# Kernel tuning notes

Hardware: AMD Instinct MI355X
Metric: run time of the kernel (lower is better)

## Reference

```python
import jax, jax.numpy as jnp
import numpy as np

CODEBOOK_SIZE = 8192
EMBED_DIM = 256


def setup_inputs() -> dict:
    key = jax.random.key(0)
    k1, k2 = jax.random.split(key)
    z = jax.random.normal(k1, (8, 4096, EMBED_DIM), dtype=jnp.float32)
    # matches torch init: uniform_(-1/codebook_size, 1/codebook_size)
    codebook = jax.random.uniform(
        k2, (CODEBOOK_SIZE, EMBED_DIM), dtype=jnp.float32,
        minval=-1.0 / CODEBOOK_SIZE, maxval=1.0 / CODEBOOK_SIZE)
    return {"z": z, "codebook": codebook}


def reference(z, codebook):
    # z: [B, S, D]; codebook: [K, D]
    z_flat = z.reshape(-1, z.shape[-1])                      # [N, D]
    # ||z||^2 - 2 z.E^T + ||E||^2  -> [N, K]
    distances = (
        jnp.sum(z_flat * z_flat, axis=1, keepdims=True)
        - 2.0 * jnp.einsum("nd,kd->nk", z_flat, codebook)
        + jnp.sum(codebook * codebook, axis=1)
    )
    encoding_indices = jnp.argmin(distances, axis=1)         # [N]
    z_q = codebook[encoding_indices].reshape(z.shape)        # [B, S, D]
    return z_q, encoding_indices
```

## Files before the change

### kernel.cpp

```cpp
#include <hip/hip_runtime.h>


#define NROWS 32768
#define DIM   256
#define KCB   8192
#define CANDCAP 128
#define MARGIN  4.5e-4f
#define WBUF    320
#define NTILE   512
#define RECB    9216

#define OFF_CAND  0
#define OFF_CNT   2097152
#define OFF_ZSQ   2129920
#define OFF_CSQ   2162688
#define OFF_OVL   2170880
#define OFF_OVC   2203648
#define OFF_IMG   2203664
#define OFF_IDX   8388608

using bf16x8 = __attribute__((ext_vector_type(8))) short;
using f32x4  = __attribute__((ext_vector_type(4))) float;

__device__ __forceinline__ unsigned short bf16rne(float f) {
    unsigned u = __float_as_uint(f);
    unsigned r = u + 0x7FFFu + ((u >> 16) & 1u);
    return (unsigned short)(r >> 16);
}

__device__ __forceinline__ void gld_lds16(const void* g, void* l) {
    __builtin_amdgcn_global_load_lds(
        (const __attribute__((address_space(1))) void*)g,
        (__attribute__((address_space(3))) void*)l, 16, 0, 0);
}

__device__ float np_sumsq_256(const float* __restrict__ p) {
#pragma clang fp contract(off)
    float blk[2];
    #pragma unroll
    for (int b = 0; b < 2; ++b) {
        const float* q = p + b * 128;
        float r[8];
        #pragma unroll
        for (int j = 0; j < 8; ++j) r[j] = __fmul_rn(q[j], q[j]);
        for (int i = 8; i < 128; i += 8) {
            #pragma unroll
            for (int j = 0; j < 8; ++j)
                r[j] = __fadd_rn(r[j], __fmul_rn(q[i + j], q[i + j]));
        }
        blk[b] = __fadd_rn(
            __fadd_rn(__fadd_rn(r[0], r[1]), __fadd_rn(r[2], r[3])),
            __fadd_rn(__fadd_rn(r[4], r[5]), __fadd_rn(r[6], r[7])));
    }
    return __fadd_rn(blk[0], blk[1]);
}

__global__ void vq_sumsq2_kernel(const float* __restrict__ z,
                                 const float* __restrict__ cb,
                                 float* __restrict__ zsq, float* __restrict__ csq) {
    int r = blockIdx.x * 256 + threadIdx.x;
    if (r < NROWS) zsq[r] = np_sumsq_256(z + (size_t)r * DIM);
    else if (r < NROWS + KCB) csq[r - NROWS] = np_sumsq_256(cb + (size_t)(r - NROWS) * DIM);
}

__global__ void vq_prepB_kernel(const float* __restrict__ cb,
                                const float* __restrict__ csq,
                                char* __restrict__ img,
                                unsigned* __restrict__ cnt, unsigned* __restrict__ ovc) {
    int t = blockIdx.x * 256 + threadIdx.x;
    if (t < NROWS) cnt[t] = 0;
    if (t == 0) *ovc = 0;
    if (t < 262144) {
        int s = t & 63, kk = (t >> 6) & 7, T = t >> 9;
        int code = T * 16 + (s >> 2), lhi = s & 3;
        const float* src = cb + (size_t)code * DIM + kk * 32 + lhi * 8;
        float4 v0 = *reinterpret_cast<const float4*>(src);
        float4 v1 = *reinterpret_cast<const float4*>(src + 4);
        uint4 o;
        o.x = (unsigned)bf16rne(v0.x) | ((unsigned)bf16rne(v0.y) << 16);
        o.y = (unsigned)bf16rne(v0.z) | ((unsigned)bf16rne(v0.w) << 16);
        o.z = (unsigned)bf16rne(v1.x) | ((unsigned)bf16rne(v1.y) << 16);
        o.w = (unsigned)bf16rne(v1.z) | ((unsigned)bf16rne(v1.w) << 16);
        *reinterpret_cast<uint4*>(img + (size_t)T * RECB + kk * 1024 + s * 16) = o;
    } else {
        int t2 = t - 262144;
        if (t2 < NTILE * 4) {
            int T = t2 >> 2, q = t2 & 3;
            float4 c = *reinterpret_cast<const float4*>(&csq[T * 16 + q * 4]);
            c.x += 1.0f; c.y += 1.0f; c.z += 1.0f; c.w += 1.0f;
            *reinterpret_cast<float4*>(img + (size_t)T * RECB + 8192 + q * 16) = c;
        }
    }
}

__global__ __launch_bounds__(512, 1) void vq_screen_kernel(
    const float* __restrict__ z, const char* __restrict__ img,
    unsigned* __restrict__ cnt, unsigned short* __restrict__ cand) {
    __shared__ __align__(16) unsigned char Bpriv[8][2][RECB];
    __shared__ unsigned runmin[128];
    __shared__ unsigned wcnt[8];
    __shared__ unsigned wbuf[8][WBUF];
    const int tid = threadIdx.x, lane = tid & 63, wid = tid >> 6;
    const int wr = wid >> 2, wc = wid & 3;
    const int l15 = lane & 15, lhi = lane >> 4;
    const int row0 = blockIdx.x * 128;
    const int tbase = wc * 128;
    unsigned char* myB = &Bpriv[wid][0][0];

    bf16x8 ah[4][8];
    #pragma unroll
    for (int m = 0; m < 4; ++m) {
        const float* zr = z + (size_t)(row0 + wr * 64 + m * 16 + l15) * DIM;
        #pragma unroll
        for (int kk = 0; kk < 8; ++kk) {
            float4 v0 = *reinterpret_cast<const float4*>(zr + kk * 32 + lhi * 8);
            float4 v1 = *reinterpret_cast<const float4*>(zr + kk * 32 + lhi * 8 + 4);
            uint4 o;
            o.x = (unsigned)bf16rne(v0.x) | ((unsigned)bf16rne(v0.y) << 16);
            o.y = (unsigned)bf16rne(v0.z) | ((unsigned)bf16rne(v0.w) << 16);
            o.z = (unsigned)bf16rne(v1.x) | ((unsigned)bf16rne(v1.y) << 16);
            o.w = (unsigned)bf16rne(v1.z) | ((unsigned)bf16rne(v1.w) << 16);
            ah[m][kk] = __builtin_bit_cast(bf16x8, o);
        }
    }

    if (tid < 128) runmin[tid] = 0x7F800000u;
    if (tid < 8) wcnt[tid] = 0;
    __syncthreads();

    f32x4 acc[4];
    #pragma unroll
    for (int m = 0; m < 4; ++m) acc[m] = (f32x4){0.f, 0.f, 0.f, 0.f};

    auto STAGE = [&](int buf, int ct) {
        const char* g = img + (size_t)(tbase + ct) * RECB + lane * 16;
        unsigned char* l = myB + buf * RECB;
        #pragma unroll
        for (int i = 0; i < 9; ++i)
            gld_lds16(g + i * 1024, l + i * 1024);
    };

    auto PUSH = [&](int lr, int code) {
        unsigned pi = atomicAdd(&wcnt[wid], 1u);
        if (pi < WBUF) wbuf[wid][pi] = ((unsigned)lr << 13) | (unsigned)code;
        else {
            int grow = row0 + lr;
            unsigned gs = atomicAdd(&cnt[grow], 1u);
            if (gs < CANDCAP) cand[(size_t)grow * CANDCAP + gs] = (unsigned short)code;
        }
    };

    STAGE(0, 0);

    for (int ct = 0; ct < 128; ++ct) {
        const int buf = ct & 1;
        if (ct < 127) {
            STAGE(buf ^ 1, ct + 1);
            asm volatile("s_waitcnt vmcnt(9)" ::: "memory");
        } else {
            asm volatile("s_waitcnt vmcnt(0)" ::: "memory");
        }
        const unsigned char* mb = myB + buf * RECB;
        const float cs1 = *reinterpret_cast<const float*>(mb + 8192 + l15 * 4);
        __builtin_amdgcn_s_setprio(1);
        #pragma unroll
        for (int kk = 0; kk < 8; ++kk) {
            bf16x8 bh = *reinterpret_cast<const bf16x8*>(mb + kk * 1024 + l15 * 64 + lhi * 16);
            #pragma unroll
            for (int m = 0; m < 4; ++m)
                acc[m] = __builtin_amdgcn_mfma_f32_16x16x32_bf16(ah[m][kk], bh, acc[m], 0, 0, 0);
        }
        __builtin_amdgcn_s_setprio(0);

        const int codeb = (tbase + ct) * 16 + l15;
        if (ct == 0) {
            #pragma unroll
            for (int m = 0; m < 4; ++m) {
                const int lr0 = wr * 64 + m * 16 + lhi * 4;
                #pragma unroll
                for (int r = 0; r < 4; ++r) {
                    float s2 = fmaf(acc[m][r], -2.0f, cs1);
                    float sm = s2;
                    sm = fminf(sm, __shfl_xor(sm, 1));
                    sm = fminf(sm, __shfl_xor(sm, 2));
                    sm = fminf(sm, __shfl_xor(sm, 4));
                    sm = fminf(sm, __shfl_xor(sm, 8));
                    if (l15 == 0) atomicMin(&runmin[lr0 + r], __float_as_uint(sm));
                    if (s2 < sm + MARGIN) PUSH(lr0 + r, codeb);
                }
                acc[m] = (f32x4){0.f, 0.f, 0.f, 0.f};
            }
        } else {
            #pragma unroll
            for (int m = 0; m < 4; ++m) {
                const int lr0 = wr * 64 + m * 16 + lhi * 4;
                uint4 rmb = *reinterpret_cast<const uint4*>(&runmin[lr0]);
                #pragma unroll
                for (int r = 0; r < 4; ++r) {
                    float s2 = fmaf(acc[m][r], -2.0f, cs1);
                    const unsigned rmu = (r == 0) ? rmb.x : (r == 1) ? rmb.y
                                        : (r == 2) ? rmb.z : rmb.w;
                    const float rm = __uint_as_float(rmu);
                    const bool cf = s2 < rm + MARGIN;
                    if (__any(cf)) {
                        if (cf) {
                            if (s2 < rm) atomicMin(&runmin[lr0 + r], __float_as_uint(s2));
                            PUSH(lr0 + r, codeb);
                        }
                    }
                }
                acc[m] = (f32x4){0.f, 0.f, 0.f, 0.f};
            }
        }
    }

    unsigned n = wcnt[wid]; if (n > WBUF) n = WBUF;
    for (unsigned e = lane; e < n; e += 64) {
        unsigned u = wbuf[wid][e];
        int row = row0 + (int)(u >> 13);
        int code = (int)(u & 8191u);
        unsigned slot = atomicAdd(&cnt[row], 1u);
        if (slot < CANDCAP) cand[(size_t)row * CANDCAP + slot] = (unsigned short)code;
    }
}

__global__ __launch_bounds__(256) void vq_exact_kernel(
    const float* __restrict__ z, const float* __restrict__ cb,
    const float* __restrict__ zsq, const float* __restrict__ csq,
    const unsigned* __restrict__ cnt, const unsigned short* __restrict__ cand,
    unsigned* __restrict__ ovl, unsigned* __restrict__ ovc,
    float* __restrict__ idxF) {
    __shared__ float zrow[4][DIM];
    const int wid = threadIdx.x >> 6, lane = threadIdx.x & 63;
    const int row = blockIdx.x * 4 + wid;

    float4 zv4 = *reinterpret_cast<const float4*>(&z[(size_t)row * DIM + lane * 4]);
    *reinterpret_cast<float4*>(&zrow[wid][lane * 4]) = zv4;
    __syncthreads();

    const unsigned c = cnt[row];
    if (c == 0 || c > CANDCAP) {
        if (lane == 0) { unsigned s = atomicAdd(ovc, 1u); ovl[s] = row; }
        return;
    }

    const float Zr = zsq[row];
    const float4* cb4 = reinterpret_cast<const float4*>(cb);
    float best = 3.4e38f;
    int   bi   = 0x7FFFFFFF;

    for (int j = lane; j < (int)c; j += 64) {
        int k = cand[(size_t)row * CANDCAP + j];
        float a = 0.0f;
        #pragma unroll 8
        for (int q = 0; q < 64; ++q) {
            float4 cv = cb4[(size_t)k * 64 + q];
            float4 zv = *reinterpret_cast<const float4*>(&zrow[wid][q * 4]);
            a = fmaf(zv.x, cv.x, a); a = fmaf(zv.y, cv.y, a);
            a = fmaf(zv.z, cv.z, a); a = fmaf(zv.w, cv.w, a);
        }
        float sv = __fadd_rn(__fsub_rn(Zr, __fmul_rn(2.0f, a)), csq[k]);
        if (sv < best || (sv == best && k < bi)) { best = sv; bi = k; }
    }
    #pragma unroll
    for (int mk = 32; mk >= 1; mk >>= 1) {
        float ov = __shfl_xor(best, mk);
        int   oi = __shfl_xor(bi, mk);
        if (ov < best || (ov == best && oi < bi)) { best = ov; bi = oi; }
    }
    if (lane == 0) idxF[row] = (float)bi;
}

__global__ __launch_bounds__(256) void vq_cleanup_kernel(
    const float* __restrict__ z, const float* __restrict__ cb,
    const float* __restrict__ zsq, const float* __restrict__ csq,
    const unsigned* __restrict__ ovl, const unsigned* __restrict__ ovc,
    float* __restrict__ idxF) {
    __shared__ float zrow[DIM];
    __shared__ float wv[4]; __shared__ int wi[4];
    const int lane = threadIdx.x & 63, wid = threadIdx.x >> 6;
    const unsigned count = *ovc;
    for (unsigned w = blockIdx.x; w < count; w += gridDim.x) {
        const int row = ovl[w];
        __syncthreads();
        *reinterpret_cast<float4*>(&zrow[threadIdx.x * 4 & (DIM - 1)]) =
            *reinterpret_cast<const float4*>(&z[(size_t)row * DIM + (threadIdx.x * 4 & (DIM - 1))]);
        __syncthreads();
        const float Zr = zsq[row];
        const float4* cb4 = reinterpret_cast<const float4*>(cb);
        float best = 3.4e38f; int bi = 0x7FFFFFFF;
        for (int k = threadIdx.x; k < KCB; k += 256) {
            float a = 0.0f;
            #pragma unroll 8
            for (int q = 0; q < 64; ++q) {
                float4 cv = cb4[(size_t)k * 64 + q];
                float4 zv = *reinterpret_cast<const float4*>(&zrow[q * 4]);
                a = fmaf(zv.x, cv.x, a); a = fmaf(zv.y, cv.y, a);
                a = fmaf(zv.z, cv.z, a); a = fmaf(zv.w, cv.w, a);
            }
            float sv = __fadd_rn(__fsub_rn(Zr, __fmul_rn(2.0f, a)), csq[k]);
            if (sv < best || (sv == best && k < bi)) { best = sv; bi = k; }
        }
        #pragma unroll
        for (int mk = 32; mk >= 1; mk >>= 1) {
            float ov = __shfl_xor(best, mk);
            int   oi = __shfl_xor(bi, mk);
            if (ov < best || (ov == best && oi < bi)) { best = ov; bi = oi; }
        }
        if (lane == 0) { wv[wid] = best; wi[wid] = bi; }
        __syncthreads();
        if (threadIdx.x == 0) {
            #pragma unroll
            for (int u = 1; u < 4; ++u)
                if (wv[u] < best || (wv[u] == best && wi[u] < bi)) { best = wv[u]; bi = wi[u]; }
            idxF[row] = (float)bi;
        }
    }
}

__global__ void vq_gather_kernel(const float* __restrict__ cb,
                                 const float* __restrict__ idxF,
                                 float4* __restrict__ out4) {
    int g = blockIdx.x * blockDim.x + threadIdx.x;
    const float4* cb4 = reinterpret_cast<const float4*>(cb);
    for (int i = g; i < NROWS * 64; i += gridDim.x * blockDim.x) {
        int row = i >> 6, q = i & 63;
        int idx = (int)idxF[row];
        out4[i] = cb4[(size_t)idx * 64 + q];
    }
}

extern "C" void kernel_launch(void* const* d_in, const int* in_sizes, int n_in,
                              void* d_out, int out_size, void* d_ws, size_t ws_size,
                              hipStream_t stream) {
    const float* z  = (const float*)d_in[0];
    const float* cb = (const float*)d_in[1];
    float* out = (float*)d_out;

    unsigned short* candp = (unsigned short*)(out + OFF_CAND);
    unsigned*       cntp  = (unsigned*)(out + OFF_CNT);
    float*          zsq   = out + OFF_ZSQ;
    float*          csq   = out + OFF_CSQ;
    unsigned*       ovl   = (unsigned*)(out + OFF_OVL);
    unsigned*       ovc   = (unsigned*)(out + OFF_OVC);
    char*           img   = (char*)(out + OFF_IMG);
    float*          idxF  = out + OFF_IDX;

    vq_sumsq2_kernel<<<(NROWS + KCB) / 256, 256, 0, stream>>>(z, cb, zsq, csq);
    vq_prepB_kernel<<<1032, 256, 0, stream>>>(cb, csq, img, cntp, ovc);
    vq_screen_kernel<<<NROWS / 128, 512, 0, stream>>>(z, img, cntp, candp);
    vq_exact_kernel<<<NROWS / 4, 256, 0, stream>>>(z, cb, zsq, csq, cntp, candp, ovl, ovc, idxF);
    vq_cleanup_kernel<<<64, 256, 0, stream>>>(z, cb, zsq, csq, ovl, ovc, idxF);
    vq_gather_kernel<<<2048, 256, 0, stream>>>(cb, idxF, (float4*)out);
}
```

Measured before the change: 351.6 us.

## Load codebook tiles straight to registers and drop the LDS staging buffers

The screening kernel stops staging bf16 codebook tiles through per-wave LDS double buffers with global_load_lds. It now loads each lane's B fragments directly into registers with a two-deep register ping-pong and software-pipelined MFMA/epilogue. The image layout is reordered so that each lane's 16-byte fragment is contiguous, and csq+1 is moved to its own array. Removing roughly 147KB of LDS allows launch bounds of two blocks per CU, raising occupancy, at the cost of more VGPR pressure and no LDS reuse across waves.

```diff
diff --git a/kernel.cpp b/kernel.cpp
--- a/kernel.cpp
+++ b/kernel.cpp
@@ -8,15 +8,15 @@
 #define MARGIN  4.5e-4f
 #define WBUF    320
 #define NTILE   512
-#define RECB    9216
 
 #define OFF_CAND  0
 #define OFF_CNT   2097152
 #define OFF_ZSQ   2129920
 #define OFF_CSQ   2162688
-#define OFF_OVL   2170880
-#define OFF_OVC   2203648
-#define OFF_IMG   2203664
+#define OFF_CSQ1  2170880
+#define OFF_OVL   2179072
+#define OFF_OVC   2211840
+#define OFF_IMG   2211856
 #define OFF_IDX   8388608
 
 using bf16x8 = __attribute__((ext_vector_type(8))) short;
@@ -26,12 +26,6 @@
     unsigned u = __float_as_uint(f);
     unsigned r = u + 0x7FFFu + ((u >> 16) & 1u);
     return (unsigned short)(r >> 16);
-}
-
-__device__ __forceinline__ void gld_lds16(const void* g, void* l) {
-    __builtin_amdgcn_global_load_lds(
-        (const __attribute__((address_space(1))) void*)g,
-        (__attribute__((address_space(3))) void*)l, 16, 0, 0);
 }
 
 __device__ float np_sumsq_256(const float* __restrict__ p) {
@@ -65,15 +59,15 @@
 
 __global__ void vq_prepB_kernel(const float* __restrict__ cb,
                                 const float* __restrict__ csq,
-                                char* __restrict__ img,
+                                char* __restrict__ img, float* __restrict__ csq1,
                                 unsigned* __restrict__ cnt, unsigned* __restrict__ ovc) {
     int t = blockIdx.x * 256 + threadIdx.x;
     if (t < NROWS) cnt[t] = 0;
     if (t == 0) *ovc = 0;
     if (t < 262144) {
         int s = t & 63, kk = (t >> 6) & 7, T = t >> 9;
-        int code = T * 16 + (s >> 2), lhi = s & 3;
-        const float* src = cb + (size_t)code * DIM + kk * 32 + lhi * 8;
+        int code = s & 15, lhi = s >> 4;
+        const float* src = cb + (size_t)(T * 16 + code) * DIM + kk * 32 + lhi * 8;
         float4 v0 = *reinterpret_cast<const float4*>(src);
         float4 v1 = *reinterpret_cast<const float4*>(src + 4);
         uint4 o;
@@ -81,22 +75,16 @@
         o.y = (unsigned)bf16rne(v0.z) | ((unsigned)bf16rne(v0.w) << 16);
         o.z = (unsigned)bf16rne(v1.x) | ((unsigned)bf16rne(v1.y) << 16);
         o.w = (unsigned)bf16rne(v1.z) | ((unsigned)bf16rne(v1.w) << 16);
-        *reinterpret_cast<uint4*>(img + (size_t)T * RECB + kk * 1024 + s * 16) = o;
-    } else {
-        int t2 = t - 262144;
-        if (t2 < NTILE * 4) {
-            int T = t2 >> 2, q = t2 & 3;
-            float4 c = *reinterpret_cast<const float4*>(&csq[T * 16 + q * 4]);
-            c.x += 1.0f; c.y += 1.0f; c.z += 1.0f; c.w += 1.0f;
-            *reinterpret_cast<float4*>(img + (size_t)T * RECB + 8192 + q * 16) = c;
-        }
-    }
-}
-
-__global__ __launch_bounds__(512, 1) void vq_screen_kernel(
+        *reinterpret_cast<uint4*>(img + (size_t)T * 8192 + kk * 1024 + s * 16) = o;
+    } else if (t < 262144 + KCB) {
+        csq1[t - 262144] = csq[t - 262144] + 1.0f;
+    }
+}
+
+__global__ __launch_bounds__(512, 2) void vq_screen_kernel(
     const float* __restrict__ z, const char* __restrict__ img,
+    const float* __restrict__ csq1,
     unsigned* __restrict__ cnt, unsigned short* __restrict__ cand) {
-    __shared__ __align__(16) unsigned char Bpriv[8][2][RECB];
     __shared__ unsigned runmin[128];
     __shared__ unsigned wcnt[8];
     __shared__ unsigned wbuf[8][WBUF];
@@ -105,7 +93,6 @@
     const int l15 = lane & 15, lhi = lane >> 4;
     const int row0 = blockIdx.x * 128;
     const int tbase = wc * 128;
-    unsigned char* myB = &Bpriv[wid][0][0];
 
     bf16x8 ah[4][8];
     #pragma unroll
@@ -132,13 +119,12 @@
     #pragma unroll
     for (int m = 0; m < 4; ++m) acc[m] = (f32x4){0.f, 0.f, 0.f, 0.f};
 
-    auto STAGE = [&](int buf, int ct) {
-        const char* g = img + (size_t)(tbase + ct) * RECB + lane * 16;
-        unsigned char* l = myB + buf * RECB;
-        #pragma unroll
-        for (int i = 0; i < 9; ++i)
-            gld_lds16(g + i * 1024, l + i * 1024);
-    };
+    const char*  gp = img + (size_t)tbase * 8192 + (size_t)lane * 16;
+    const float* cp = csq1 + tbase * 16 + l15;
+    int codeb = tbase * 16 + l15;
+
+    uint4 bA[8]; float csA;
+    uint4 bB[8]; float csB;
 
     auto PUSH = [&](int lr, int code) {
         unsigned pi = atomicAdd(&wcnt[wid], 1u);
@@ -150,68 +136,87 @@
         }
     };
 
-    STAGE(0, 0);
-
-    for (int ct = 0; ct < 128; ++ct) {
-        const int buf = ct & 1;
-        if (ct < 127) {
-            STAGE(buf ^ 1, ct + 1);
-            asm volatile("s_waitcnt vmcnt(9)" ::: "memory");
-        } else {
-            asm volatile("s_waitcnt vmcnt(0)" ::: "memory");
-        }
-        const unsigned char* mb = myB + buf * RECB;
-        const float cs1 = *reinterpret_cast<const float*>(mb + 8192 + l15 * 4);
-        __builtin_amdgcn_s_setprio(1);
+#define LOADR(bh, cs)                                                     \
+    {                                                                     \
+        _Pragma("unroll")                                                 \
+        for (int kk = 0; kk < 8; ++kk)                                    \
+            bh[kk] = *reinterpret_cast<const uint4*>(gp + kk * 1024);     \
+        cs = *cp;                                                         \
+        gp += 8192; cp += 16;                                             \
+    }
+
+#define MFMAS(bh)                                                         \
+    {                                                                     \
+        __builtin_amdgcn_s_setprio(1);                                    \
+        _Pragma("unroll")                                                 \
+        for (int kk = 0; kk < 8; ++kk) {                                  \
+            bf16x8 bhv = __builtin_bit_cast(bf16x8, bh[kk]);              \
+            _Pragma("unroll")                                             \
+            for (int m = 0; m < 4; ++m)                                   \
+                acc[m] = __builtin_amdgcn_mfma_f32_16x16x32_bf16(         \
+                    ah[m][kk], bhv, acc[m], 0, 0, 0);                     \
+        }                                                                 \
+        __builtin_amdgcn_s_setprio(0);                                    \
+    }
+
+#define EPI(csv)                                                          \
+    {                                                                     \
+        _Pragma("unroll")                                                 \
+        for (int m = 0; m < 4; ++m) {                                     \
+            const int lr0 = wr * 64 + m * 16 + lhi * 4;                   \
+            uint4 rmb = *reinterpret_cast<const uint4*>(&runmin[lr0]);    \
+            float s0 = fmaf(acc[m][0], -2.0f, csv);                       \
+            float s1 = fmaf(acc[m][1], -2.0f, csv);                       \
+            float s2 = fmaf(acc[m][2], -2.0f, csv);                       \
+            float s3 = fmaf(acc[m][3], -2.0f, csv);                       \
+            bool c0 = s0 < __uint_as_float(rmb.x) + MARGIN;               \
+            bool c1 = s1 < __uint_as_float(rmb.y) + MARGIN;               \
+            bool c2 = s2 < __uint_as_float(rmb.z) + MARGIN;               \
+            bool c3 = s3 < __uint_as_float(rmb.w) + MARGIN;               \
+            if (__any(c0 | c1 | c2 | c3)) {                               \
+                if (c0) { if (s0 < __uint_as_float(rmb.x)) atomicMin(&runmin[lr0 + 0], __float_as_uint(s0)); PUSH(lr0 + 0, codeb); } \
+                if (c1) { if (s1 < __uint_as_float(rmb.y)) atomicMin(&runmin[lr0 + 1], __float_as_uint(s1)); PUSH(lr0 + 1, codeb); } \
+                if (c2) { if (s2 < __uint_as_float(rmb.z)) atomicMin(&runmin[lr0 + 2], __float_as_uint(s2)); PUSH(lr0 + 2, codeb); } \
+                if (c3) { if (s3 < __uint_as_float(rmb.w)) atomicMin(&runmin[lr0 + 3], __float_as_uint(s3)); PUSH(lr0 + 3, codeb); } \
+            }                                                             \
+            acc[m] = (f32x4){0.f, 0.f, 0.f, 0.f};                         \
+        }                                                                 \
+        codeb += 16;                                                      \
+    }
+
+    LOADR(bA, csA);
+    LOADR(bB, csB);
+    MFMAS(bA);
+    {
         #pragma unroll
-        for (int kk = 0; kk < 8; ++kk) {
-            bf16x8 bh = *reinterpret_cast<const bf16x8*>(mb + kk * 1024 + l15 * 64 + lhi * 16);
+        for (int m = 0; m < 4; ++m) {
+            const int lr0 = wr * 64 + m * 16 + lhi * 4;
             #pragma unroll
-            for (int m = 0; m < 4; ++m)
-                acc[m] = __builtin_amdgcn_mfma_f32_16x16x32_bf16(ah[m][kk], bh, acc[m], 0, 0, 0);
-        }
-        __builtin_amdgcn_s_setprio(0);
-
-        const int codeb = (tbase + ct) * 16 + l15;
-        if (ct == 0) {
-            #pragma unroll
-            for (int m = 0; m < 4; ++m) {
-                const int lr0 = wr * 64 + m * 16 + lhi * 4;
-                #pragma unroll
-                for (int r = 0; r < 4; ++r) {
-                    float s2 = fmaf(acc[m][r], -2.0f, cs1);
-                    float sm = s2;
-                    sm = fminf(sm, __shfl_xor(sm, 1));
-                    sm = fminf(sm, __shfl_xor(sm, 2));
-                    sm = fminf(sm, __shfl_xor(sm, 4));
-                    sm = fminf(sm, __shfl_xor(sm, 8));
-                    if (l15 == 0) atomicMin(&runmin[lr0 + r], __float_as_uint(sm));
-                    if (s2 < sm + MARGIN) PUSH(lr0 + r, codeb);
-                }
-                acc[m] = (f32x4){0.f, 0.f, 0.f, 0.f};
+            for (int r = 0; r < 4; ++r) {
+                float s2 = fmaf(acc[m][r], -2.0f, csA);
+                float sm = s2;
+                sm = fminf(sm, __shfl_xor(sm, 1));
+                sm = fminf(sm, __shfl_xor(sm, 2));
+                sm = fminf(sm, __shfl_xor(sm, 4));
+                sm = fminf(sm, __shfl_xor(sm, 8));
+                if (l15 == 0) atomicMin(&runmin[lr0 + r], __float_as_uint(sm));
+                if (s2 < sm + MARGIN) PUSH(lr0 + r, codeb);
             }
-        } else {
-            #pragma unroll
-            for (int m = 0; m < 4; ++m) {
-                const int lr0 = wr * 64 + m * 16 + lhi * 4;
-                uint4 rmb = *reinterpret_cast<const uint4*>(&runmin[lr0]);
-                #pragma unroll
-                for (int r = 0; r < 4; ++r) {
-                    float s2 = fmaf(acc[m][r], -2.0f, cs1);
-                    const unsigned rmu = (r == 0) ? rmb.x : (r == 1) ? rmb.y
-                                        : (r == 2) ? rmb.z : rmb.w;
-                    const float rm = __uint_as_float(rmu);
-                    const bool cf = s2 < rm + MARGIN;
-                    if (__any(cf)) {
-                        if (cf) {
-                            if (s2 < rm) atomicMin(&runmin[lr0 + r], __float_as_uint(s2));
-                            PUSH(lr0 + r, codeb);
-                        }
-                    }
-                }
-                acc[m] = (f32x4){0.f, 0.f, 0.f, 0.f};
-            }
-        }
+            acc[m] = (f32x4){0.f, 0.f, 0.f, 0.f};
+        }
+        codeb += 16;
+    }
+    LOADR(bA, csA);
+    MFMAS(bB);
+    EPI(csB);
+
+    for (int ct = 2; ct < 128; ct += 2) {
+        LOADR(bB, csB);
+        MFMAS(bA);
+        EPI(csA);
+        LOADR(bA, csA);
+        MFMAS(bB);
+        EPI(csB);
     }
 
     unsigned n = wcnt[wid]; if (n > WBUF) n = WBUF;
@@ -222,6 +227,9 @@
         unsigned slot = atomicAdd(&cnt[row], 1u);
         if (slot < CANDCAP) cand[(size_t)row * CANDCAP + slot] = (unsigned short)code;
     }
+#undef LOADR
+#undef MFMAS
+#undef EPI
 }
 
 __global__ __launch_bounds__(256) void vq_exact_kernel(
@@ -341,14 +349,15 @@
     unsigned*       cntp  = (unsigned*)(out + OFF_CNT);
     float*          zsq   = out + OFF_ZSQ;
     float*          csq   = out + OFF_CSQ;
+    float*          csq1  = out + OFF_CSQ1;
     unsigned*       ovl   = (unsigned*)(out + OFF_OVL);
     unsigned*       ovc   = (unsigned*)(out + OFF_OVC);
     char*           img   = (char*)(out + OFF_IMG);
     float*          idxF  = out + OFF_IDX;
 
     vq_sumsq2_kernel<<<(NROWS + KCB) / 256, 256, 0, stream>>>(z, cb, zsq, csq);
-    vq_prepB_kernel<<<1032, 256, 0, stream>>>(cb, csq, img, cntp, ovc);
-    vq_screen_kernel<<<NROWS / 128, 512, 0, stream>>>(z, img, cntp, candp);
+    vq_prepB_kernel<<<1057, 256, 0, stream>>>(cb, csq, img, csq1, cntp, ovc);
+    vq_screen_kernel<<<NROWS / 128, 512, 0, stream>>>(z, img, csq1, cntp, candp);
     vq_exact_kernel<<<NROWS / 4, 256, 0, stream>>>(z, cb, zsq, csq, cntp, candp, ovl, ovc, idxF);
     vq_cleanup_kernel<<<64, 256, 0, stream>>>(z, cb, zsq, csq, ovl, ovc, idxF);
     vq_gather_kernel<<<2048, 256, 0, stream>>>(cb, idxF, (float4*)out);
```

After: 299.0 us. 1.18x faster.
